# Optimization experiments

Measured on AMD Instinct MI355X. Metric: run time of the kernel, lower is better.

Reference implementation:

```python
import jax, jax.numpy as jnp
import numpy as np

N, E, F_IN, F_EDGE, HID, OUT = 100000, 1600000, 128, 8, 128, 2
BN_EPS = 1e-5


def setup_inputs() -> dict:
    key = jax.random.key(0)
    ks = jax.random.split(key, 16)
    rn = lambda k, shape, s=0.05: jax.random.normal(k, shape, jnp.float32) * s
    return {
        "x": jax.random.normal(ks[0], (N, F_IN), jnp.float32),
        "edge_attr": jax.random.uniform(ks[1], (E, F_EDGE), dtype=jnp.float32),
        "edge_index": jax.random.randint(ks[2], (2, E), 0, N, jnp.int32),
        # edge MLP: Linear(F_EDGE, HID) -> ReLU -> Linear(HID, 1) -> Sigmoid
        "ew1_w": rn(ks[3], (F_EDGE, HID)), "ew1_b": jnp.zeros((HID,), jnp.float32),
        "ew2_w": rn(ks[4], (HID, 1)), "ew2_b": jnp.zeros((1,), jnp.float32),
        # SAGEConv layers: lin_l (on aggregated neighbors, with bias) + lin_r (root)
        "w1_l": rn(ks[5], (F_IN, HID)), "b1_l": jnp.zeros((HID,), jnp.float32), "w1_r": rn(ks[6], (F_IN, HID)),
        "w2_l": rn(ks[7], (HID, HID)), "b2_l": jnp.zeros((HID,), jnp.float32), "w2_r": rn(ks[8], (HID, HID)),
        "w3_l": rn(ks[9], (HID, OUT)), "b3_l": jnp.zeros((OUT,), jnp.float32), "w3_r": rn(ks[10], (HID, OUT)),
        # BatchNorm1d (eval mode: running stats)
        "bn1_g": jnp.ones((HID,), jnp.float32), "bn1_b": jnp.zeros((HID,), jnp.float32),
        "bn1_m": rn(ks[11], (HID,), 0.01), "bn1_v": jnp.ones((HID,), jnp.float32),
        "bn2_g": jnp.ones((HID,), jnp.float32), "bn2_b": jnp.zeros((HID,), jnp.float32),
        "bn2_m": rn(ks[12], (HID,), 0.01), "bn2_v": jnp.ones((HID,), jnp.float32),
    }


def _sage(x, src, dst, ew, w_l, b_l, w_r):
    # PyG SAGEConv(aggr='mean'): msg = x[src] * edge_weight, mean over incoming edges at dst
    msg = x[src] * ew[:, None]                                  # [E, F]
    s = jax.ops.segment_sum(msg, dst, num_segments=N)           # [N, F]
    deg = jax.ops.segment_sum(jnp.ones((src.shape[0],), x.dtype), dst, num_segments=N)
    agg = s / jnp.maximum(deg, 1.0)[:, None]
    return agg @ w_l + b_l + x @ w_r


def _bn_eval(h, g, b, m, v):
    return (h - m) * jax.lax.rsqrt(v + BN_EPS) * g + b


def reference(x, edge_attr, edge_index,
              ew1_w, ew1_b, ew2_w, ew2_b,
              w1_l, b1_l, w1_r, w2_l, b2_l, w2_r, w3_l, b3_l, w3_r,
              bn1_g, bn1_b, bn1_m, bn1_v, bn2_g, bn2_b, bn2_m, bn2_v):
    src, dst = edge_index[0], edge_index[1]
    # per-edge scalar weight from small MLP
    ew = jax.nn.sigmoid(jax.nn.relu(edge_attr @ ew1_w + ew1_b) @ ew2_w + ew2_b).reshape(-1)
    h = _sage(x, src, dst, ew, w1_l, b1_l, w1_r)
    h = jax.nn.relu(_bn_eval(h, bn1_g, bn1_b, bn1_m, bn1_v))    # dropout no-op in eval
    h = _sage(h, src, dst, ew, w2_l, b2_l, w2_r)
    h = jax.nn.relu(_bn_eval(h, bn2_g, bn2_b, bn2_m, bn2_v))
    return _sage(h, src, dst, ew, w3_l, b3_l, w3_r)
```

## Files before the change

kernel.cpp:

```cpp
#include <hip/hip_runtime.h>
#include <math.h>

#define N_NODES 100000
#define N_EDGES 1600000
#define F_INF   128
#define HIDF    128

#define MLP_BLOCKS  2048
#define CAST_BLOCKS 12500
#define WP_BASE     (CAST_BLOCKS + MLP_BLOCKS)
#define FRONT_GRID  (WP_BASE + 256)

typedef __attribute__((ext_vector_type(8)))  short short8;
typedef __attribute__((ext_vector_type(16))) float floatx16;

__device__ __forceinline__ unsigned short f2bf(float f) {
    unsigned u = __float_as_uint(f);
    return (unsigned short)((u + 0x7FFFu + ((u >> 16) & 1u)) >> 16);
}
__device__ __forceinline__ float bf2f(unsigned short h) {
    return __uint_as_float((unsigned)h << 16);
}

__global__ __launch_bounds__(256) void k_front(
        const float* __restrict__ x,
        unsigned short* __restrict__ xbHi, unsigned short* __restrict__ xbLo,
        const int* __restrict__ dst, int* __restrict__ deg,
        unsigned char* __restrict__ rank,
        const float* __restrict__ ea,
        const float* __restrict__ mw1, const float* __restrict__ mb1,
        const float* __restrict__ mw2, const float* __restrict__ mb2,
        float* __restrict__ ew,
        const float* __restrict__ w1l, const float* __restrict__ w1r,
        short* __restrict__ W1hi, short* __restrict__ W1lo,
        const float* __restrict__ w2l, const float* __restrict__ w2r,
        short* __restrict__ W2hi, short* __restrict__ W2lo) {
    const int bid = blockIdx.x;

    if (bid >= WP_BASE) {
        const int wb  = bid - WP_BASE;
        const int idx = (wb & 127) * 256 + threadIdx.x;
        const float* Wl = (wb < 128) ? w1l : w2l;
        const float* Wr = (wb < 128) ? w1r : w2r;
        short* Whi = (wb < 128) ? W1hi : W2hi;
        short* Wlo = (wb < 128) ? W1lo : W2lo;
        const int j  = idx & 7;
        const int L  = (idx >> 3) & 63;
        const int cb = (idx >> 9) & 3;
        const int kb = (idx >> 11);
        const int k  = kb * 16 + (L >> 5) * 8 + j;
        const int n  = cb * 32 + (L & 31);
        const float a = (k < 128) ? Wl[k * 128 + n] : Wr[(k - 128) * 128 + n];
        const unsigned short hb = f2bf(a);
        Whi[idx] = (short)hb;
        Wlo[idx] = (short)f2bf(a - bf2f(hb));
        return;
    }

    const bool is_mlp = ((bid % 7) == 3) && (bid < 7 * MLP_BLOCKS);
    if (!is_mlp) {
        const int c   = (bid < 4) ? 0 : min(MLP_BLOCKS, (bid - 4) / 7 + 1);
        const int gid = (bid - c) * 256 + (int)threadIdx.x;
        const int i   = gid * 4;
        const float4 v = *(const float4*)(x + i);
        ushort4 h, l;
        h.x = f2bf(v.x); l.x = f2bf(v.x - bf2f(h.x));
        h.y = f2bf(v.y); l.y = f2bf(v.y - bf2f(h.y));
        h.z = f2bf(v.z); l.z = f2bf(v.z - bf2f(h.z));
        h.w = f2bf(v.w); l.w = f2bf(v.w - bf2f(h.w));
        *(ushort4*)(xbHi + i) = h;
        *(ushort4*)(xbLo + i) = l;
        if ((gid & 1) == 0) {
            const int e = gid >> 1;
            rank[e] = (unsigned char)atomicAdd(&deg[dst[e]], 1);
        }
        return;
    }

    const int lane = threadIdx.x & 63;
    const int cl   = lane & 31;
    const int half = lane >> 5;
    const int wid  = (bid / 7) * 4 + ((int)threadIdx.x >> 6);
    const int nw   = MLP_BLOCKS * 4;

    short8 bw[4];
    float  w2c[4];
#pragma unroll
    for (int cb = 0; cb < 4; ++cb) {
        const int n = cb * 32 + cl;
        short8 b;
        if (half == 0) {
#pragma unroll
            for (int j = 0; j < 8; ++j) b[j] = (short)f2bf(mw1[j * 128 + n]);
        } else {
            b[0] = (short)f2bf(mb1[n]);
#pragma unroll
            for (int j = 1; j < 8; ++j) b[j] = 0;
        }
        bw[cb] = b;
        w2c[cb] = mw2[n];
    }
    short8 Abias;
    Abias[0] = (short)0x3F80;
#pragma unroll
    for (int j = 1; j < 8; ++j) Abias[j] = 0;

    floatx16 czero;
#pragma unroll
    for (int r = 0; r < 16; ++r) czero[r] = 0.f;

    const float bias2 = mb2[0];

    for (int e0 = wid * 32; e0 < N_EDGES; e0 += nw * 32) {
        short8 Ah;
        if (half == 0) {
            const float4 a0 = *(const float4*)(ea + (size_t)(e0 + cl) * 8);
            const float4 a1 = *(const float4*)(ea + (size_t)(e0 + cl) * 8 + 4);
            Ah[0] = (short)f2bf(a0.x); Ah[1] = (short)f2bf(a0.y);
            Ah[2] = (short)f2bf(a0.z); Ah[3] = (short)f2bf(a0.w);
            Ah[4] = (short)f2bf(a1.x); Ah[5] = (short)f2bf(a1.y);
            Ah[6] = (short)f2bf(a1.z); Ah[7] = (short)f2bf(a1.w);
        } else {
            Ah = Abias;
        }

        float z[16];
#pragma unroll
        for (int r = 0; r < 16; ++r) z[r] = 0.f;

#pragma unroll
        for (int cb = 0; cb < 4; ++cb) {
            floatx16 acc = __builtin_amdgcn_mfma_f32_32x32x16_bf16(Ah, bw[cb], czero, 0, 0, 0);
#pragma unroll
            for (int r = 0; r < 16; ++r)
                z[r] = fmaf(fmaxf(acc[r], 0.f), w2c[cb], z[r]);
        }

#pragma unroll
        for (int m = 1; m <= 16; m <<= 1) {
#pragma unroll
            for (int r = 0; r < 16; ++r) z[r] += __shfl_xor(z[r], m, 64);
        }

        float zz = z[0];
#pragma unroll
        for (int r = 1; r < 16; ++r) zz = (cl == r) ? z[r] : zz;
        if (cl < 16) {
            const int row = (cl & 3) + 8 * (cl >> 2) + 4 * half;
            ew[e0 + row] = 1.f / (1.f + __expf(-(zz + bias2)));
        }
    }
}

__global__ void k_scan1(const int* __restrict__ deg, int* __restrict__ incl,
                        int* __restrict__ bsum) {
    __shared__ int sm[1024];
    const int tid = threadIdx.x;
    const int gi  = blockIdx.x * 1024 + tid;
    int v = (gi < N_NODES) ? deg[gi] : 0;
    sm[tid] = v;
    __syncthreads();
    for (int off = 1; off < 1024; off <<= 1) {
        int t = (tid >= off) ? sm[tid - off] : 0;
        __syncthreads();
        sm[tid] += t;
        __syncthreads();
    }
    if (gi < N_NODES) incl[gi] = sm[tid];
    if (tid == 1023) bsum[blockIdx.x] = sm[1023];
}

__global__ void k_scan23(const int* __restrict__ incl, const int* __restrict__ bsum,
                         int* __restrict__ rowptr, int nb) {
    __shared__ int sm[128];
    const int tid = threadIdx.x;
    int v = 0;
    if (tid < 128) {
        v = (tid < nb) ? bsum[tid] : 0;
        sm[tid] = v;
    }
    __syncthreads();
    for (int off = 1; off < 128; off <<= 1) {
        int t = 0;
        if (tid < 128 && tid >= off) t = sm[tid - off];
        __syncthreads();
        if (tid < 128) sm[tid] += t;
        __syncthreads();
    }
    if (tid < 128) sm[tid] -= v;
    __syncthreads();
    const int i = blockIdx.x * 256 + tid;
    if (i < N_NODES) rowptr[i + 1] = sm[i >> 10] + incl[i];
    if (i == 0) rowptr[0] = 0;
}

__global__ void k_fill(const int* __restrict__ src, const int* __restrict__ dst,
                       const float* __restrict__ ew, const int* __restrict__ rowptr,
                       const unsigned char* __restrict__ rank,
                       unsigned* __restrict__ cw) {
    int e = blockIdx.x * 256 + threadIdx.x;
    if (e < N_EDGES) {
        int d   = dst[e];
        int pos = rowptr[d] + (int)rank[e];
        unsigned wb = (unsigned)f2bf(ew[e]) & 0x7FFFu;
        cw[pos] = ((unsigned)src[e] << 15) | wb;
    }
}

__global__ __launch_bounds__(256) void k_agg16(
        const unsigned short* __restrict__ xb, const int* __restrict__ rowptr,
        const unsigned* __restrict__ cw,
        unsigned short* __restrict__ aggHi, unsigned short* __restrict__ aggLo) {
    const int lane = threadIdx.x & 63;
    const int half = lane >> 5;
    const int cl   = lane & 31;
    const int node = blockIdx.x * (blockDim.x >> 6) + (threadIdx.x >> 6);
    if (node >= N_NODES) return;
    const int s = rowptr[node], e = rowptr[node + 1];
    float a0 = 0.f, a1 = 0.f, a2 = 0.f, a3 = 0.f;

    for (int j0 = s; j0 < e; j0 += 8) {
        int ss[4]; float ww[4];
#pragma unroll
        for (int u = 0; u < 4; ++u) {
            const int j  = j0 + 2 * u + half;
            const int jc = min(j, e - 1);
            const unsigned p = cw[jc];
            ss[u] = (int)(p >> 15);
            ww[u] = (j < e) ? __uint_as_float((p & 0x7FFFu) << 16) : 0.f;
        }
        uint2 g[4];
#pragma unroll
        for (int u = 0; u < 4; ++u)
            g[u] = *(const uint2*)(xb + (size_t)ss[u] * 128 + cl * 4);
#pragma unroll
        for (int u = 0; u < 4; ++u) {
            const float f0 = __uint_as_float(g[u].x << 16);
            const float f1 = __uint_as_float(g[u].x & 0xFFFF0000u);
            const float f2 = __uint_as_float(g[u].y << 16);
            const float f3 = __uint_as_float(g[u].y & 0xFFFF0000u);
            a0 = fmaf(ww[u], f0, a0);
            a1 = fmaf(ww[u], f1, a1);
            a2 = fmaf(ww[u], f2, a2);
            a3 = fmaf(ww[u], f3, a3);
        }
    }
    a0 += __shfl_xor(a0, 32, 64);
    a1 += __shfl_xor(a1, 32, 64);
    a2 += __shfl_xor(a2, 32, 64);
    a3 += __shfl_xor(a3, 32, 64);
    if (half == 0) {
        const float inv = 1.f / fmaxf((float)(e - s), 1.f);
        a0 *= inv; a1 *= inv; a2 *= inv; a3 *= inv;
        ushort4 h, l;
        h.x = f2bf(a0); l.x = f2bf(a0 - bf2f(h.x));
        h.y = f2bf(a1); l.y = f2bf(a1 - bf2f(h.y));
        h.z = f2bf(a2); l.z = f2bf(a2 - bf2f(h.z));
        h.w = f2bf(a3); l.w = f2bf(a3 - bf2f(h.w));
        *(ushort4*)(aggHi + (size_t)node * 128 + cl * 4) = h;
        *(ushort4*)(aggLo + (size_t)node * 128 + cl * 4) = l;
    }
}

__global__ __launch_bounds__(256) void k_gemm(
    const unsigned short* __restrict__ AaggHi, const unsigned short* __restrict__ AaggLo,
    const unsigned short* __restrict__ AxHi, const unsigned short* __restrict__ AxLo,
    const short* __restrict__ Whi, const short* __restrict__ Wlo,
    const float* __restrict__ bl,
    const float* __restrict__ bng, const float* __restrict__ bnb,
    const float* __restrict__ bnm, const float* __restrict__ bnv,
    unsigned short* __restrict__ outHi, unsigned short* __restrict__ outLo) {
    const int tid  = threadIdx.x;
    const int lane = tid & 63;
    const int w    = tid >> 6;
    const int row0 = blockIdx.x * 128 + w * 32;
    const int rrow = lane & 31;
    const int kq   = lane >> 5;
    const int arow = min(row0 + rrow, N_NODES - 1);

    floatx16 acc[4];
#pragma unroll
    for (int cb = 0; cb < 4; ++cb)
#pragma unroll
        for (int r = 0; r < 16; ++r) acc[cb][r] = 0.f;

    const size_t abase = (size_t)arow * 128 + kq * 8;

#pragma unroll 2
    for (int kb = 0; kb < 16; ++kb) {
        const size_t ao = abase + (kb & 7) * 16;
        const short8 Ah = *(const short8*)(((kb < 8) ? AaggHi : AxHi) + ao);
        const short8 Al = *(const short8*)(((kb < 8) ? AaggLo : AxLo) + ao);
#pragma unroll
        for (int cb = 0; cb < 4; ++cb) {
            const size_t wo = ((size_t)(kb * 4 + cb) * 64 + lane) * 8;
            const short8 wh = *(const short8*)(Whi + wo);
            const short8 wl = *(const short8*)(Wlo + wo);
            acc[cb] = __builtin_amdgcn_mfma_f32_32x32x16_bf16(Ah, wh, acc[cb], 0, 0, 0);
            acc[cb] = __builtin_amdgcn_mfma_f32_32x32x16_bf16(Al, wh, acc[cb], 0, 0, 0);
            acc[cb] = __builtin_amdgcn_mfma_f32_32x32x16_bf16(Ah, wl, acc[cb], 0, 0, 0);
        }
    }

#pragma unroll
    for (int cb = 0; cb < 4; ++cb) {
        const int c = cb * 32 + (lane & 31);
        const float s = bng[c] * rsqrtf(bnv[c] + 1e-5f);
        const float t = (bl[c] - bnm[c]) * s + bnb[c];
#pragma unroll
        for (int r = 0; r < 16; ++r) {
            const int row = row0 + (r & 3) + 8 * (r >> 2) + 4 * kq;
            if (row < N_NODES) {
                const float v = fmaxf(fmaf(acc[cb][r], s, t), 0.f);
                const unsigned short hb = f2bf(v);
                outHi[(size_t)row * 128 + c] = hb;
                outLo[(size_t)row * 128 + c] = f2bf(v - bf2f(hb));
            }
        }
    }
}

__global__ void k_lin3(const unsigned short* __restrict__ hHi,
                       const unsigned short* __restrict__ hLo,
                       const float* __restrict__ w3l,
                       const float* __restrict__ w3r, float* __restrict__ t4) {
    const int lane = threadIdx.x & 63;
    const int node = blockIdx.x * (blockDim.x >> 6) + (threadIdx.x >> 6);
    if (node >= N_NODES) return;
    const size_t b = (size_t)node * 128;
    const float h0 = bf2f(hHi[b + lane])      + bf2f(hLo[b + lane]);
    const float h1 = bf2f(hHi[b + 64 + lane]) + bf2f(hLo[b + 64 + lane]);
    const float2 wl0 = *(const float2*)(w3l + lane * 2);
    const float2 wl1 = *(const float2*)(w3l + (64 + lane) * 2);
    const float2 wr0 = *(const float2*)(w3r + lane * 2);
    const float2 wr1 = *(const float2*)(w3r + (64 + lane) * 2);
    float p0 = h0 * wl0.x + h1 * wl1.x;
    float p1 = h0 * wl0.y + h1 * wl1.y;
    float p2 = h0 * wr0.x + h1 * wr1.x;
    float p3 = h0 * wr0.y + h1 * wr1.y;
#pragma unroll
    for (int m = 1; m < 64; m <<= 1) {
        p0 += __shfl_xor(p0, m, 64);
        p1 += __shfl_xor(p1, m, 64);
        p2 += __shfl_xor(p2, m, 64);
        p3 += __shfl_xor(p3, m, 64);
    }
    if (lane == 0) {
        float4 o; o.x = p0; o.y = p1; o.z = p2; o.w = p3;
        *(float4*)(t4 + (size_t)node * 4) = o;
    }
}

__global__ void k_out(const float* __restrict__ t4, const int* __restrict__ rowptr,
                      const unsigned* __restrict__ cw,
                      const float* __restrict__ b3, float* __restrict__ out) {
    const int lane = threadIdx.x & 63;
    const int node = blockIdx.x * (blockDim.x >> 6) + (threadIdx.x >> 6);
    if (node >= N_NODES) return;
    const int s = rowptr[node], e = rowptr[node + 1];
    float a0 = 0.f, a1 = 0.f;
    for (int j = s + lane; j < e; j += 64) {
        const unsigned p = cw[j];
        const int   sr = (int)(p >> 15);
        const float w  = __uint_as_float((p & 0x7FFFu) << 16);
        float2 t = *(const float2*)(t4 + (size_t)sr * 4);
        a0 += w * t.x; a1 += w * t.y;
    }
#pragma unroll
    for (int m = 1; m < 64; m <<= 1) {
        a0 += __shfl_xor(a0, m, 64);
        a1 += __shfl_xor(a1, m, 64);
    }
    if (lane == 0) {
        float inv = 1.f / fmaxf((float)(e - s), 1.f);
        float2 o;
        o.x = a0 * inv + b3[0] + t4[(size_t)node * 4 + 2];
        o.y = a1 * inv + b3[1] + t4[(size_t)node * 4 + 3];
        *(float2*)(out + (size_t)node * 2) = o;
    }
}

extern "C" void kernel_launch(void* const* d_in, const int* in_sizes, int n_in,
                              void* d_out, int out_size, void* d_ws, size_t ws_size,
                              hipStream_t stream) {
    const float* x    = (const float*)d_in[0];
    const float* ea   = (const float*)d_in[1];
    const int*   ei   = (const int*)d_in[2];
    const float* ew1w = (const float*)d_in[3];
    const float* ew1b = (const float*)d_in[4];
    const float* ew2w = (const float*)d_in[5];
    const float* ew2b = (const float*)d_in[6];
    const float* w1l  = (const float*)d_in[7];
    const float* b1l  = (const float*)d_in[8];
    const float* w1r  = (const float*)d_in[9];
    const float* w2l  = (const float*)d_in[10];
    const float* b2l  = (const float*)d_in[11];
    const float* w2r  = (const float*)d_in[12];
    const float* w3l  = (const float*)d_in[13];
    const float* b3l  = (const float*)d_in[14];
    const float* w3r  = (const float*)d_in[15];
    const float* bn1g = (const float*)d_in[16];
    const float* bn1b = (const float*)d_in[17];
    const float* bn1m = (const float*)d_in[18];
    const float* bn1v = (const float*)d_in[19];
    const float* bn2g = (const float*)d_in[20];
    const float* bn2b = (const float*)d_in[21];
    const float* bn2m = (const float*)d_in[22];
    const float* bn2v = (const float*)d_in[23];

    const int* src = ei;
    const int* dst = ei + N_EDGES;
    float* out = (float*)d_out;

    size_t off = 0;
    auto carve = [&](size_t bytes) -> void* {
        void* p = (char*)d_ws + off;
        off += (bytes + 255) & ~(size_t)255;
        return p;
    };
    float* ew     = (float*)carve((size_t)N_EDGES * 4);
    unsigned* cw  = (unsigned*)carve((size_t)N_EDGES * 4);
    unsigned char* rank = (unsigned char*)carve((size_t)N_EDGES);
    int*   rowptr = (int*)carve((size_t)(N_NODES + 1) * 4);
    int*   deg    = (int*)carve((size_t)N_NODES * 4);
    int*   bsum   = (int*)carve(128 * 4);
    int*   incl   = (int*)carve((size_t)N_NODES * 4);
    float* t4     = (float*)carve((size_t)N_NODES * 4 * 4);
    short* W1hi   = (short*)carve(32768 * 2);
    short* W1lo   = (short*)carve(32768 * 2);
    short* W2hi   = (short*)carve(32768 * 2);
    short* W2lo   = (short*)carve(32768 * 2);
    unsigned short* xbHi  = (unsigned short*)carve((size_t)N_NODES * 128 * 2);
    unsigned short* xbLo  = (unsigned short*)carve((size_t)N_NODES * 128 * 2);
    unsigned short* aggHi = (unsigned short*)carve((size_t)N_NODES * 128 * 2);
    unsigned short* aggLo = (unsigned short*)carve((size_t)N_NODES * 128 * 2);
    unsigned short* hHi   = (unsigned short*)carve((size_t)N_NODES * 128 * 2);
    unsigned short* hLo   = (unsigned short*)carve((size_t)N_NODES * 128 * 2);
    unsigned short* hBhi  = (unsigned short*)carve((size_t)N_NODES * 128 * 2);
    unsigned short* hBlo  = (unsigned short*)carve((size_t)N_NODES * 128 * 2);
    (void)ws_size; (void)n_in; (void)in_sizes; (void)out_size;

    hipMemsetAsync(deg, 0, (size_t)N_NODES * 4, stream);

    const int EB = (N_EDGES + 255) / 256;
    const int NB_SCAN = (N_NODES + 1023) / 1024;
    const int NWB = (N_NODES + 3) / 4;
    const int GB = (N_NODES + 127) / 128;

    k_front<<<FRONT_GRID, 256, 0, stream>>>(
        x, xbHi, xbLo, dst, deg, rank,
        ea, ew1w, ew1b, ew2w, ew2b, ew,
        w1l, w1r, W1hi, W1lo, w2l, w2r, W2hi, W2lo);
    k_scan1<<<NB_SCAN, 1024, 0, stream>>>(deg, incl, bsum);
    k_scan23<<<(N_NODES + 255) / 256, 256, 0, stream>>>(incl, bsum, rowptr, NB_SCAN);
    k_fill<<<EB, 256, 0, stream>>>(src, dst, ew, rowptr, rank, cw);

    k_agg16<<<NWB, 256, 0, stream>>>(xbHi, rowptr, cw, aggHi, aggLo);
    k_gemm<<<GB, 256, 0, stream>>>(aggHi, aggLo, xbHi, xbLo, W1hi, W1lo, b1l,
                                   bn1g, bn1b, bn1m, bn1v, hHi, hLo);
    k_agg16<<<NWB, 256, 0, stream>>>(hHi, rowptr, cw, aggHi, aggLo);
    k_gemm<<<GB, 256, 0, stream>>>(aggHi, aggLo, hHi, hLo, W2hi, W2lo, b2l,
                                   bn2g, bn2b, bn2m, bn2v, hBhi, hBlo);
    k_lin3<<<NWB, 256, 0, stream>>>(hBhi, hBlo, w3l, w3r, t4);
    k_out<<<NWB, 256, 0, stream>>>(t4, rowptr, cw, b3l, out);
}
```

Measured before the change: 562.6 us.

## Stage A tiles in swizzled LDS and split GEMM columns across waves

The GEMM kernel now processes 32 rows per block instead of 128. Each of the four waves computes one 32-column slice, and the A rows (agg and root, hi and lo) are staged into XOR-swizzled shared memory with coalesced 16-byte loads. This removes the per-wave strided global loads of A and cuts accumulator registers from four floatx16 to one, which should raise occupancy and give 4x more blocks. The cost is extra LDS traffic and barriers, and row bounds checks are dropped on the assumption that N divides evenly by 32.

```diff
diff --git a/kernel.cpp b/kernel.cpp
--- a/kernel.cpp
+++ b/kernel.cpp
@@ -270,53 +270,85 @@
     const float* __restrict__ bng, const float* __restrict__ bnb,
     const float* __restrict__ bnm, const float* __restrict__ bnv,
     unsigned short* __restrict__ outHi, unsigned short* __restrict__ outLo) {
+    __shared__ unsigned short SH[32 * 128];
+    __shared__ unsigned short SL[32 * 128];
     const int tid  = threadIdx.x;
     const int lane = tid & 63;
-    const int w    = tid >> 6;
-    const int row0 = blockIdx.x * 128 + w * 32;
+    const int cb   = tid >> 6;
     const int rrow = lane & 31;
     const int kq   = lane >> 5;
-    const int arow = min(row0 + rrow, N_NODES - 1);
-
-    floatx16 acc[4];
-#pragma unroll
-    for (int cb = 0; cb < 4; ++cb)
-#pragma unroll
-        for (int r = 0; r < 16; ++r) acc[cb][r] = 0.f;
-
-    const size_t abase = (size_t)arow * 128 + kq * 8;
-
-#pragma unroll 2
-    for (int kb = 0; kb < 16; ++kb) {
-        const size_t ao = abase + (kb & 7) * 16;
-        const short8 Ah = *(const short8*)(((kb < 8) ? AaggHi : AxHi) + ao);
-        const short8 Al = *(const short8*)(((kb < 8) ? AaggLo : AxLo) + ao);
-#pragma unroll
-        for (int cb = 0; cb < 4; ++cb) {
-            const size_t wo = ((size_t)(kb * 4 + cb) * 64 + lane) * 8;
-            const short8 wh = *(const short8*)(Whi + wo);
-            const short8 wl = *(const short8*)(Wlo + wo);
-            acc[cb] = __builtin_amdgcn_mfma_f32_32x32x16_bf16(Ah, wh, acc[cb], 0, 0, 0);
-            acc[cb] = __builtin_amdgcn_mfma_f32_32x32x16_bf16(Al, wh, acc[cb], 0, 0, 0);
-            acc[cb] = __builtin_amdgcn_mfma_f32_32x32x16_bf16(Ah, wl, acc[cb], 0, 0, 0);
-        }
-    }
-
-#pragma unroll
-    for (int cb = 0; cb < 4; ++cb) {
-        const int c = cb * 32 + (lane & 31);
-        const float s = bng[c] * rsqrtf(bnv[c] + 1e-5f);
-        const float t = (bl[c] - bnm[c]) * s + bnb[c];
-#pragma unroll
-        for (int r = 0; r < 16; ++r) {
-            const int row = row0 + (r & 3) + 8 * (r >> 2) + 4 * kq;
-            if (row < N_NODES) {
-                const float v = fmaxf(fmaf(acc[cb][r], s, t), 0.f);
-                const unsigned short hb = f2bf(v);
-                outHi[(size_t)row * 128 + c] = hb;
-                outLo[(size_t)row * 128 + c] = f2bf(v - bf2f(hb));
-            }
-        }
+    const int row0 = blockIdx.x * 32;
+
+    const int sr = tid >> 3;
+    const int sc = (tid & 7) * 16;
+    const int s0 = sc >> 3;
+    const size_t gsrc = (size_t)(row0 + sr) * 128 + sc;
+    const int ld0 = sr * 128 + ((s0 + 0) ^ (sr & 15)) * 8;
+    const int ld1 = sr * 128 + ((s0 + 1) ^ (sr & 15)) * 8;
+
+    const uint4 ah0 = *(const uint4*)(AaggHi + gsrc);
+    const uint4 ah1 = *(const uint4*)(AaggHi + gsrc + 8);
+    const uint4 al0 = *(const uint4*)(AaggLo + gsrc);
+    const uint4 al1 = *(const uint4*)(AaggLo + gsrc + 8);
+    const uint4 rh0 = *(const uint4*)(AxHi + gsrc);
+    const uint4 rh1 = *(const uint4*)(AxHi + gsrc + 8);
+    const uint4 rl0 = *(const uint4*)(AxLo + gsrc);
+    const uint4 rl1 = *(const uint4*)(AxLo + gsrc + 8);
+
+    *(uint4*)(SH + ld0) = ah0;
+    *(uint4*)(SH + ld1) = ah1;
+    *(uint4*)(SL + ld0) = al0;
+    *(uint4*)(SL + ld1) = al1;
+
+    floatx16 acc;
+#pragma unroll
+    for (int r = 0; r < 16; ++r) acc[r] = 0.f;
+
+    __syncthreads();
+
+#pragma unroll
+    for (int kb = 0; kb < 8; ++kb) {
+        const int slot = (2 * kb + kq) ^ (rrow & 15);
+        const short8 Ah = *(const short8*)(SH + rrow * 128 + slot * 8);
+        const short8 Al = *(const short8*)(SL + rrow * 128 + slot * 8);
+        const size_t wo = ((size_t)(kb * 4 + cb) * 64 + lane) * 8;
+        const short8 wh = *(const short8*)(Whi + wo);
+        const short8 wl = *(const short8*)(Wlo + wo);
+        acc = __builtin_amdgcn_mfma_f32_32x32x16_bf16(Ah, wh, acc, 0, 0, 0);
+        acc = __builtin_amdgcn_mfma_f32_32x32x16_bf16(Al, wh, acc, 0, 0, 0);
+        acc = __builtin_amdgcn_mfma_f32_32x32x16_bf16(Ah, wl, acc, 0, 0, 0);
+    }
+
+    __syncthreads();
+    *(uint4*)(SH + ld0) = rh0;
+    *(uint4*)(SH + ld1) = rh1;
+    *(uint4*)(SL + ld0) = rl0;
+    *(uint4*)(SL + ld1) = rl1;
+    __syncthreads();
+
+#pragma unroll
+    for (int kb = 0; kb < 8; ++kb) {
+        const int slot = (2 * kb + kq) ^ (rrow & 15);
+        const short8 Ah = *(const short8*)(SH + rrow * 128 + slot * 8);
+        const short8 Al = *(const short8*)(SL + rrow * 128 + slot * 8);
+        const size_t wo = ((size_t)((kb + 8) * 4 + cb) * 64 + lane) * 8;
+        const short8 wh = *(const short8*)(Whi + wo);
+        const short8 wl = *(const short8*)(Wlo + wo);
+        acc = __builtin_amdgcn_mfma_f32_32x32x16_bf16(Ah, wh, acc, 0, 0, 0);
+        acc = __builtin_amdgcn_mfma_f32_32x32x16_bf16(Al, wh, acc, 0, 0, 0);
+        acc = __builtin_amdgcn_mfma_f32_32x32x16_bf16(Ah, wl, acc, 0, 0, 0);
+    }
+
+    const int c = cb * 32 + rrow;
+    const float s = bng[c] * rsqrtf(bnv[c] + 1e-5f);
+    const float t = (bl[c] - bnm[c]) * s + bnb[c];
+#pragma unroll
+    for (int r = 0; r < 16; ++r) {
+        const int row = row0 + (r & 3) + 8 * (r >> 2) + 4 * kq;
+        const float v = fmaxf(fmaf(acc[r], s, t), 0.f);
+        const unsigned short hb = f2bf(v);
+        outHi[(size_t)row * 128 + c] = hb;
+        outLo[(size_t)row * 128 + c] = f2bf(v - bf2f(hb));
     }
 }
 
@@ -445,7 +477,7 @@
     const int EB = (N_EDGES + 255) / 256;
     const int NB_SCAN = (N_NODES + 1023) / 1024;
     const int NWB = (N_NODES + 3) / 4;
-    const int GB = (N_NODES + 127) / 128;
+    const int GB = N_NODES / 32;
 
     k_front<<<FRONT_GRID, 256, 0, stream>>>(
         x, xbHi, xbLo, dst, deg, rank,
```

New measurement: 525.7 us. 6.6% less time.

## Fuse neighbor aggregation into GEMM via LDS and fold layer-3 linear into layer-2

Applied to the files above, without the earlier changes.

Each block now aggregates 32 nodes' neighbor features directly into swizzled LDS tiles (hi/lo bf16 split) and runs the MFMA GEMM from LDS, removing the global agg buffers and separate aggregation kernels. The second fused kernel also stages the BN/ReLU output in LDS and computes the final 128->4 projection with MFMA, eliminating k_lin3 and the hB buffers. This saves global round trips and launches. In exchange each block has fewer waves doing the latency-bound gather, one wave per 8 nodes, and a mostly-idle MFMA for the tiny projection.

```diff
diff --git a/kernel.cpp b/kernel.cpp
--- a/kernel.cpp
+++ b/kernel.cpp
@@ -207,147 +207,200 @@
     }
 }
 
-__global__ __launch_bounds__(256) void k_agg16(
-        const unsigned short* __restrict__ xb, const int* __restrict__ rowptr,
-        const unsigned* __restrict__ cw,
-        unsigned short* __restrict__ aggHi, unsigned short* __restrict__ aggLo) {
-    const int lane = threadIdx.x & 63;
-    const int half = lane >> 5;
-    const int cl   = lane & 31;
-    const int node = blockIdx.x * (blockDim.x >> 6) + (threadIdx.x >> 6);
-    if (node >= N_NODES) return;
-    const int s = rowptr[node], e = rowptr[node + 1];
-    float a0 = 0.f, a1 = 0.f, a2 = 0.f, a3 = 0.f;
-
-    for (int j0 = s; j0 < e; j0 += 8) {
-        int ss[4]; float ww[4];
-#pragma unroll
-        for (int u = 0; u < 4; ++u) {
-            const int j  = j0 + 2 * u + half;
-            const int jc = min(j, e - 1);
-            const unsigned p = cw[jc];
-            ss[u] = (int)(p >> 15);
-            ww[u] = (j < e) ? __uint_as_float((p & 0x7FFFu) << 16) : 0.f;
-        }
-        uint2 g[4];
-#pragma unroll
-        for (int u = 0; u < 4; ++u)
-            g[u] = *(const uint2*)(xb + (size_t)ss[u] * 128 + cl * 4);
-#pragma unroll
-        for (int u = 0; u < 4; ++u) {
-            const float f0 = __uint_as_float(g[u].x << 16);
-            const float f1 = __uint_as_float(g[u].x & 0xFFFF0000u);
-            const float f2 = __uint_as_float(g[u].y << 16);
-            const float f3 = __uint_as_float(g[u].y & 0xFFFF0000u);
-            a0 = fmaf(ww[u], f0, a0);
-            a1 = fmaf(ww[u], f1, a1);
-            a2 = fmaf(ww[u], f2, a2);
-            a3 = fmaf(ww[u], f3, a3);
-        }
-    }
-    a0 += __shfl_xor(a0, 32, 64);
-    a1 += __shfl_xor(a1, 32, 64);
-    a2 += __shfl_xor(a2, 32, 64);
-    a3 += __shfl_xor(a3, 32, 64);
-    if (half == 0) {
-        const float inv = 1.f / fmaxf((float)(e - s), 1.f);
-        a0 *= inv; a1 *= inv; a2 *= inv; a3 *= inv;
-        ushort4 h, l;
-        h.x = f2bf(a0); l.x = f2bf(a0 - bf2f(h.x));
-        h.y = f2bf(a1); l.y = f2bf(a1 - bf2f(h.y));
-        h.z = f2bf(a2); l.z = f2bf(a2 - bf2f(h.z));
-        h.w = f2bf(a3); l.w = f2bf(a3 - bf2f(h.w));
-        *(ushort4*)(aggHi + (size_t)node * 128 + cl * 4) = h;
-        *(ushort4*)(aggLo + (size_t)node * 128 + cl * 4) = l;
-    }
-}
-
-__global__ __launch_bounds__(256) void k_gemm(
-    const unsigned short* __restrict__ AaggHi, const unsigned short* __restrict__ AaggLo,
-    const unsigned short* __restrict__ AxHi, const unsigned short* __restrict__ AxLo,
+#define GEMM_BODY(tabHi, tabLo)                                                  \
+    const int tid  = threadIdx.x;                                                \
+    const int lane = tid & 63;                                                   \
+    const int cb   = tid >> 6;                                                   \
+    const int half = lane >> 5;                                                  \
+    const int cl   = lane & 31;                                                  \
+    const int rrow = cl;                                                         \
+    const int kq   = half;                                                       \
+    const int row0 = blockIdx.x * 32;                                            \
+    for (int i = 0; i < 8; ++i) {                                                \
+        const int nl = cb * 8 + i;                                               \
+        const int node = row0 + nl;                                              \
+        const int s = rowptr[node], e = rowptr[node + 1];                        \
+        float a0 = 0.f, a1 = 0.f, a2 = 0.f, a3 = 0.f;                            \
+        for (int j0 = s; j0 < e; j0 += 8) {                                      \
+            int ss[4]; float ww[4];                                              \
+            _Pragma("unroll")                                                    \
+            for (int u = 0; u < 4; ++u) {                                        \
+                const int j  = j0 + 2 * u + half;                                \
+                const int jc = min(j, e - 1);                                    \
+                const unsigned p = cw[jc];                                       \
+                ss[u] = (int)(p >> 15);                                          \
+                ww[u] = (j < e) ? __uint_as_float((p & 0x7FFFu) << 16) : 0.f;    \
+            }                                                                    \
+            uint2 g[4];                                                          \
+            _Pragma("unroll")                                                    \
+            for (int u = 0; u < 4; ++u)                                          \
+                g[u] = *(const uint2*)(tabHi + (size_t)ss[u] * 128 + cl * 4);    \
+            _Pragma("unroll")                                                    \
+            for (int u = 0; u < 4; ++u) {                                        \
+                const float f0 = __uint_as_float(g[u].x << 16);                  \
+                const float f1 = __uint_as_float(g[u].x & 0xFFFF0000u);          \
+                const float f2 = __uint_as_float(g[u].y << 16);                  \
+                const float f3 = __uint_as_float(g[u].y & 0xFFFF0000u);          \
+                a0 = fmaf(ww[u], f0, a0);                                        \
+                a1 = fmaf(ww[u], f1, a1);                                        \
+                a2 = fmaf(ww[u], f2, a2);                                        \
+                a3 = fmaf(ww[u], f3, a3);                                        \
+            }                                                                    \
+        }                                                                        \
+        a0 += __shfl_xor(a0, 32, 64);                                            \
+        a1 += __shfl_xor(a1, 32, 64);                                            \
+        a2 += __shfl_xor(a2, 32, 64);                                            \
+        a3 += __shfl_xor(a3, 32, 64);                                            \
+        const float inv = 1.f / fmaxf((float)(e - s), 1.f);                      \
+        a0 *= inv; a1 *= inv; a2 *= inv; a3 *= inv;                              \
+        unsigned short v0, v1, v2, v3;                                           \
+        if (half == 0) {                                                         \
+            v0 = f2bf(a0); v1 = f2bf(a1); v2 = f2bf(a2); v3 = f2bf(a3);          \
+        } else {                                                                 \
+            const unsigned short h0 = f2bf(a0), h1 = f2bf(a1),                   \
+                                 h2 = f2bf(a2), h3 = f2bf(a3);                   \
+            v0 = f2bf(a0 - bf2f(h0)); v1 = f2bf(a1 - bf2f(h1));                  \
+            v2 = f2bf(a2 - bf2f(h2)); v3 = f2bf(a3 - bf2f(h3));                  \
+        }                                                                        \
+        uint2 wv;                                                                \
+        wv.x = (unsigned)v0 | ((unsigned)v1 << 16);                              \
+        wv.y = (unsigned)v2 | ((unsigned)v3 << 16);                              \
+        unsigned short* const myLds = half ? SL : SH;                            \
+        *(uint2*)(myLds + nl * 128 + ((cl >> 1) ^ (nl & 15)) * 8                 \
+                  + (cl & 1) * 4) = wv;                                          \
+    }                                                                            \
+    const int sr = tid >> 3;                                                     \
+    const int s0 = (tid & 7) * 2;                                                \
+    const size_t gsrc = (size_t)(row0 + sr) * 128 + (tid & 7) * 16;              \
+    const int ld0 = sr * 128 + ((s0 + 0) ^ (sr & 15)) * 8;                       \
+    const int ld1 = sr * 128 + ((s0 + 1) ^ (sr & 15)) * 8;                       \
+    const uint4 rh0 = *(const uint4*)(tabHi + gsrc);                             \
+    const uint4 rh1 = *(const uint4*)(tabHi + gsrc + 8);                         \
+    const uint4 rl0 = *(const uint4*)(tabLo + gsrc);                             \
+    const uint4 rl1 = *(const uint4*)(tabLo + gsrc + 8);                         \
+    floatx16 acc;                                                                \
+    _Pragma("unroll")                                                            \
+    for (int r = 0; r < 16; ++r) acc[r] = 0.f;                                   \
+    __syncthreads();                                                             \
+    _Pragma("unroll")                                                            \
+    for (int kb = 0; kb < 8; ++kb) {                                             \
+        const int slot = (2 * kb + kq) ^ (rrow & 15);                            \
+        const short8 Ah = *(const short8*)(SH + rrow * 128 + slot * 8);          \
+        const short8 Al = *(const short8*)(SL + rrow * 128 + slot * 8);          \
+        const size_t wo = ((size_t)(kb * 4 + cb) * 64 + lane) * 8;               \
+        const short8 wh = *(const short8*)(Whi + wo);                            \
+        const short8 wl = *(const short8*)(Wlo + wo);                            \
+        acc = __builtin_amdgcn_mfma_f32_32x32x16_bf16(Ah, wh, acc, 0, 0, 0);     \
+        acc = __builtin_amdgcn_mfma_f32_32x32x16_bf16(Al, wh, acc, 0, 0, 0);     \
+        acc = __builtin_amdgcn_mfma_f32_32x32x16_bf16(Ah, wl, acc, 0, 0, 0);     \
+    }                                                                            \
+    __syncthreads();                                                             \
+    *(uint4*)(SH + ld0) = rh0;                                                   \
+    *(uint4*)(SH + ld1) = rh1;                                                   \
+    *(uint4*)(SL + ld0) = rl0;                                                   \
+    *(uint4*)(SL + ld1) = rl1;                                                   \
+    __syncthreads();                                                             \
+    _Pragma("unroll")                                                            \
+    for (int kb = 0; kb < 8; ++kb) {                                             \
+        const int slot = (2 * kb + kq) ^ (rrow & 15);                            \
+        const short8 Ah = *(const short8*)(SH + rrow * 128 + slot * 8);          \
+        const short8 Al = *(const short8*)(SL + rrow * 128 + slot * 8);          \
+        const size_t wo = ((size_t)((kb + 8) * 4 + cb) * 64 + lane) * 8;         \
+        const short8 wh = *(const short8*)(Whi + wo);                            \
+        const short8 wl = *(const short8*)(Wlo + wo);                            \
+        acc = __builtin_amdgcn_mfma_f32_32x32x16_bf16(Ah, wh, acc, 0, 0, 0);     \
+        acc = __builtin_amdgcn_mfma_f32_32x32x16_bf16(Al, wh, acc, 0, 0, 0);     \
+        acc = __builtin_amdgcn_mfma_f32_32x32x16_bf16(Ah, wl, acc, 0, 0, 0);     \
+    }
+
+__global__ __launch_bounds__(256) void k_fused1(
+    const unsigned short* __restrict__ tHi, const unsigned short* __restrict__ tLo,
+    const int* __restrict__ rowptr, const unsigned* __restrict__ cw,
     const short* __restrict__ Whi, const short* __restrict__ Wlo,
     const float* __restrict__ bl,
     const float* __restrict__ bng, const float* __restrict__ bnb,
     const float* __restrict__ bnm, const float* __restrict__ bnv,
     unsigned short* __restrict__ outHi, unsigned short* __restrict__ outLo) {
-    const int tid  = threadIdx.x;
-    const int lane = tid & 63;
-    const int w    = tid >> 6;
-    const int row0 = blockIdx.x * 128 + w * 32;
-    const int rrow = lane & 31;
-    const int kq   = lane >> 5;
-    const int arow = min(row0 + rrow, N_NODES - 1);
-
-    floatx16 acc[4];
-#pragma unroll
-    for (int cb = 0; cb < 4; ++cb)
-#pragma unroll
-        for (int r = 0; r < 16; ++r) acc[cb][r] = 0.f;
-
-    const size_t abase = (size_t)arow * 128 + kq * 8;
-
-#pragma unroll 2
-    for (int kb = 0; kb < 16; ++kb) {
-        const size_t ao = abase + (kb & 7) * 16;
-        const short8 Ah = *(const short8*)(((kb < 8) ? AaggHi : AxHi) + ao);
-        const short8 Al = *(const short8*)(((kb < 8) ? AaggLo : AxLo) + ao);
-#pragma unroll
-        for (int cb = 0; cb < 4; ++cb) {
-            const size_t wo = ((size_t)(kb * 4 + cb) * 64 + lane) * 8;
-            const short8 wh = *(const short8*)(Whi + wo);
-            const short8 wl = *(const short8*)(Wlo + wo);
-            acc[cb] = __builtin_amdgcn_mfma_f32_32x32x16_bf16(Ah, wh, acc[cb], 0, 0, 0);
-            acc[cb] = __builtin_amdgcn_mfma_f32_32x32x16_bf16(Al, wh, acc[cb], 0, 0, 0);
-            acc[cb] = __builtin_amdgcn_mfma_f32_32x32x16_bf16(Ah, wl, acc[cb], 0, 0, 0);
-        }
-    }
-
-#pragma unroll
-    for (int cb = 0; cb < 4; ++cb) {
-        const int c = cb * 32 + (lane & 31);
-        const float s = bng[c] * rsqrtf(bnv[c] + 1e-5f);
-        const float t = (bl[c] - bnm[c]) * s + bnb[c];
-#pragma unroll
-        for (int r = 0; r < 16; ++r) {
-            const int row = row0 + (r & 3) + 8 * (r >> 2) + 4 * kq;
-            if (row < N_NODES) {
-                const float v = fmaxf(fmaf(acc[cb][r], s, t), 0.f);
-                const unsigned short hb = f2bf(v);
-                outHi[(size_t)row * 128 + c] = hb;
-                outLo[(size_t)row * 128 + c] = f2bf(v - bf2f(hb));
+    __shared__ unsigned short SH[32 * 128];
+    __shared__ unsigned short SL[32 * 128];
+    GEMM_BODY(tHi, tLo)
+
+    const int c = cb * 32 + rrow;
+    const float s = bng[c] * rsqrtf(bnv[c] + 1e-5f);
+    const float t = (bl[c] - bnm[c]) * s + bnb[c];
+#pragma unroll
+    for (int r = 0; r < 16; ++r) {
+        const int row = row0 + (r & 3) + 8 * (r >> 2) + 4 * kq;
+        const float v = fmaxf(fmaf(acc[r], s, t), 0.f);
+        const unsigned short hb = f2bf(v);
+        outHi[(size_t)row * 128 + c] = hb;
+        outLo[(size_t)row * 128 + c] = f2bf(v - bf2f(hb));
+    }
+}
+
+__global__ __launch_bounds__(256) void k_fused2(
+    const unsigned short* __restrict__ tHi, const unsigned short* __restrict__ tLo,
+    const int* __restrict__ rowptr, const unsigned* __restrict__ cw,
+    const short* __restrict__ Whi, const short* __restrict__ Wlo,
+    const float* __restrict__ bl,
+    const float* __restrict__ bng, const float* __restrict__ bnb,
+    const float* __restrict__ bnm, const float* __restrict__ bnv,
+    const float* __restrict__ w3l, const float* __restrict__ w3r,
+    float* __restrict__ t4) {
+    __shared__ unsigned short SH[32 * 128];
+    __shared__ unsigned short SL[32 * 128];
+    GEMM_BODY(tHi, tLo)
+
+    const int c = cb * 32 + rrow;
+    const float s = bng[c] * rsqrtf(bnv[c] + 1e-5f);
+    const float t = (bl[c] - bnm[c]) * s + bnb[c];
+    __syncthreads();
+#pragma unroll
+    for (int r = 0; r < 16; ++r) {
+        const int rl = (r & 3) + 8 * (r >> 2) + 4 * kq;
+        const float v = fmaxf(fmaf(acc[r], s, t), 0.f);
+        const unsigned short hb = f2bf(v);
+        const int sl = ((c >> 3) ^ (rl & 15)) * 8 + (c & 7);
+        SH[rl * 128 + sl] = hb;
+        SL[rl * 128 + sl] = f2bf(v - bf2f(hb));
+    }
+    __syncthreads();
+
+    if (tid < 64) {
+        const int n = rrow;
+        floatx16 a2;
+#pragma unroll
+        for (int r = 0; r < 16; ++r) a2[r] = 0.f;
+#pragma unroll
+        for (int kb = 0; kb < 8; ++kb) {
+            const int slot = (2 * kb + kq) ^ (rrow & 15);
+            const short8 Ah = *(const short8*)(SH + rrow * 128 + slot * 8);
+            const short8 Al = *(const short8*)(SL + rrow * 128 + slot * 8);
+            short8 Bh, Bl;
+            if (n < 4) {
+#pragma unroll
+                for (int j = 0; j < 8; ++j) {
+                    const int k = kb * 16 + kq * 8 + j;
+                    const float f = (n < 2) ? w3l[k * 2 + n] : w3r[k * 2 + (n - 2)];
+                    const unsigned short hb2 = f2bf(f);
+                    Bh[j] = (short)hb2;
+                    Bl[j] = (short)f2bf(f - bf2f(hb2));
+                }
+            } else {
+#pragma unroll
+                for (int j = 0; j < 8; ++j) { Bh[j] = 0; Bl[j] = 0; }
             }
-        }
-    }
-}
-
-__global__ void k_lin3(const unsigned short* __restrict__ hHi,
-                       const unsigned short* __restrict__ hLo,
-                       const float* __restrict__ w3l,
-                       const float* __restrict__ w3r, float* __restrict__ t4) {
-    const int lane = threadIdx.x & 63;
-    const int node = blockIdx.x * (blockDim.x >> 6) + (threadIdx.x >> 6);
-    if (node >= N_NODES) return;
-    const size_t b = (size_t)node * 128;
-    const float h0 = bf2f(hHi[b + lane])      + bf2f(hLo[b + lane]);
-    const float h1 = bf2f(hHi[b + 64 + lane]) + bf2f(hLo[b + 64 + lane]);
-    const float2 wl0 = *(const float2*)(w3l + lane * 2);
-    const float2 wl1 = *(const float2*)(w3l + (64 + lane) * 2);
-    const float2 wr0 = *(const float2*)(w3r + lane * 2);
-    const float2 wr1 = *(const float2*)(w3r + (64 + lane) * 2);
-    float p0 = h0 * wl0.x + h1 * wl1.x;
-    float p1 = h0 * wl0.y + h1 * wl1.y;
-    float p2 = h0 * wr0.x + h1 * wr1.x;
-    float p3 = h0 * wr0.y + h1 * wr1.y;
-#pragma unroll
-    for (int m = 1; m < 64; m <<= 1) {
-        p0 += __shfl_xor(p0, m, 64);
-        p1 += __shfl_xor(p1, m, 64);
-        p2 += __shfl_xor(p2, m, 64);
-        p3 += __shfl_xor(p3, m, 64);
-    }
-    if (lane == 0) {
-        float4 o; o.x = p0; o.y = p1; o.z = p2; o.w = p3;
-        *(float4*)(t4 + (size_t)node * 4) = o;
+            a2 = __builtin_amdgcn_mfma_f32_32x32x16_bf16(Ah, Bh, a2, 0, 0, 0);
+            a2 = __builtin_amdgcn_mfma_f32_32x32x16_bf16(Al, Bh, a2, 0, 0, 0);
+            a2 = __builtin_amdgcn_mfma_f32_32x32x16_bf16(Ah, Bl, a2, 0, 0, 0);
+        }
+        if (n < 4) {
+#pragma unroll
+            for (int r = 0; r < 16; ++r) {
+                const int row = row0 + (r & 3) + 8 * (r >> 2) + 4 * kq;
+                t4[(size_t)row * 4 + n] = a2[r];
+            }
+        }
     }
 }
 
@@ -432,12 +485,8 @@
     short* W2lo   = (short*)carve(32768 * 2);
     unsigned short* xbHi  = (unsigned short*)carve((size_t)N_NODES * 128 * 2);
     unsigned short* xbLo  = (unsigned short*)carve((size_t)N_NODES * 128 * 2);
-    unsigned short* aggHi = (unsigned short*)carve((size_t)N_NODES * 128 * 2);
-    unsigned short* aggLo = (unsigned short*)carve((size_t)N_NODES * 128 * 2);
     unsigned short* hHi   = (unsigned short*)carve((size_t)N_NODES * 128 * 2);
     unsigned short* hLo   = (unsigned short*)carve((size_t)N_NODES * 128 * 2);
-    unsigned short* hBhi  = (unsigned short*)carve((size_t)N_NODES * 128 * 2);
-    unsigned short* hBlo  = (unsigned short*)carve((size_t)N_NODES * 128 * 2);
     (void)ws_size; (void)n_in; (void)in_sizes; (void)out_size;
 
     hipMemsetAsync(deg, 0, (size_t)N_NODES * 4, stream);
@@ -445,7 +494,7 @@
     const int EB = (N_EDGES + 255) / 256;
     const int NB_SCAN = (N_NODES + 1023) / 1024;
     const int NWB = (N_NODES + 3) / 4;
-    const int GB = (N_NODES + 127) / 128;
+    const int GB = N_NODES / 32;
 
     k_front<<<FRONT_GRID, 256, 0, stream>>>(
         x, xbHi, xbLo, dst, deg, rank,
@@ -455,12 +504,9 @@
     k_scan23<<<(N_NODES + 255) / 256, 256, 0, stream>>>(incl, bsum, rowptr, NB_SCAN);
     k_fill<<<EB, 256, 0, stream>>>(src, dst, ew, rowptr, rank, cw);
 
-    k_agg16<<<NWB, 256, 0, stream>>>(xbHi, rowptr, cw, aggHi, aggLo);
-    k_gemm<<<GB, 256, 0, stream>>>(aggHi, aggLo, xbHi, xbLo, W1hi, W1lo, b1l,
-                                   bn1g, bn1b, bn1m, bn1v, hHi, hLo);
-    k_agg16<<<NWB, 256, 0, stream>>>(hHi, rowptr, cw, aggHi, aggLo);
-    k_gemm<<<GB, 256, 0, stream>>>(aggHi, aggLo, hHi, hLo, W2hi, W2lo, b2l,
-                                   bn2g, bn2b, bn2m, bn2v, hBhi, hBlo);
-    k_lin3<<<NWB, 256, 0, stream>>>(hBhi, hBlo, w3l, w3r, t4);
+    k_fused1<<<GB, 256, 0, stream>>>(xbHi, xbLo, rowptr, cw, W1hi, W1lo, b1l,
+                                     bn1g, bn1b, bn1m, bn1v, hHi, hLo);
+    k_fused2<<<GB, 256, 0, stream>>>(hHi, hLo, rowptr, cw, W2hi, W2lo, b2l,
+                                     bn2g, bn2b, bn2m, bn2v, w3l, w3r, t4);
     k_out<<<NWB, 256, 0, stream>>>(t4, rowptr, cw, b3l, out);
 }
```

New measurement: 509.3 us. 1.1x faster.
